# Performance work log

Measured on AMD Instinct MI355X. Metric: run time of the kernel, lower is better.

## Reference

```python
import jax, jax.numpy as jnp
import numpy as np

B, T, INPUT_DIM = 4, 2048, 1024
N_HEADS, HEAD_DIM, EMB_DIM = 16, 64, 1024


def setup_inputs() -> dict:
    key = jax.random.key(0)
    ks = jax.random.split(key, 7)
    s = 0.02
    return {
        "k": jax.random.normal(ks[0], (B, T, INPUT_DIM), jnp.float32),
        "q": jax.random.normal(ks[1], (B, T, INPUT_DIM), jnp.float32),
        "v": jax.random.normal(ks[2], (B, T, INPUT_DIM), jnp.float32),
        # weights stored [in, out] (torch Linear applies x @ W.T with W [out,in])
        "w_key": jax.random.normal(ks[3], (INPUT_DIM, N_HEADS * HEAD_DIM), jnp.float32) * s,
        "w_query": jax.random.normal(ks[4], (INPUT_DIM, N_HEADS * HEAD_DIM), jnp.float32) * s,
        "w_value": jax.random.normal(ks[5], (INPUT_DIM, N_HEADS * HEAD_DIM), jnp.float32) * s,
        "w_proj": jax.random.normal(ks[6], (N_HEADS * HEAD_DIM, EMB_DIM), jnp.float32) * s,
    }


def reference(k, q, v, w_key, w_query, w_value, w_proj):
    temperature = np.sqrt(HEAD_DIM).astype(np.float32)
    # projections -> [B, T, H, D]
    kh = (k @ w_key).reshape(B, T, N_HEADS, HEAD_DIM)
    qh = (q @ w_query).reshape(B, T, N_HEADS, HEAD_DIM)
    vh = (v @ w_value).reshape(B, T, N_HEADS, HEAD_DIM)
    # scaled dot-product attention: scores [B, H, T, T]
    scores = jnp.einsum("bqhd,bkhd->bhqk", qh, kh) / temperature
    attn = jax.nn.softmax(scores, axis=-1)
    out = jnp.einsum("bhqk,bkhd->bqhd", attn, vh).reshape(B, T, N_HEADS * HEAD_DIM)
    return out @ w_proj
```

## Files before the change

kernel.cpp:

```cpp
#include <hip/hip_runtime.h>

typedef unsigned short bf16_t;
typedef __attribute__((ext_vector_type(8))) short short8;
typedef __attribute__((ext_vector_type(4))) float f32x4;
typedef __attribute__((ext_vector_type(16))) float f32x16;
typedef __attribute__((ext_vector_type(4))) unsigned short usx4;

#define T_SEQ 2048
#define NHEAD 16

__device__ __forceinline__ unsigned short f2bf(float x) {
  union { float f; unsigned u; } v; v.f = x;
  unsigned r = v.u + 0x7fffu + ((v.u >> 16) & 1u);
  return (unsigned short)(r >> 16);
}

__device__ __forceinline__ void gld_lds16(const void* g, void* l) {
  __builtin_amdgcn_global_load_lds((const __attribute__((address_space(1))) void*)g,
                                   (__attribute__((address_space(3))) void*)l, 16, 0, 0);
}

__global__ __launch_bounds__(256) void cvt_bf16(const float* __restrict__ in,
                                                bf16_t* __restrict__ out, int n4) {
  int i = blockIdx.x * 256 + threadIdx.x;
  const int stride = gridDim.x * 256;
  for (; i < n4; i += stride) {
    const float4 v = ((const float4*)in)[i];
    usx4 w = { f2bf(v.x), f2bf(v.y), f2bf(v.z), f2bf(v.w) };
    ((usx4*)out)[i] = w;
  }
}

__global__ __launch_bounds__(256) void wtrans(const float* __restrict__ w0, const float* __restrict__ w1,
                                              const float* __restrict__ w2, const float* __restrict__ w3,
                                              bf16_t* __restrict__ wt) {
  __shared__ float tile[32][33];
  const float* w = (blockIdx.z == 0) ? w0 : (blockIdx.z == 1) ? w1 : (blockIdx.z == 2) ? w2 : w3;
  bf16_t* o = wt + (size_t)blockIdx.z * 1024 * 1024;
  const int c = threadIdx.x & 31;
  const int r = threadIdx.x >> 5;
  const int k0 = blockIdx.y * 32, n0 = blockIdx.x * 32;
#pragma unroll
  for (int rr = 0; rr < 32; rr += 8)
    tile[r + rr][c] = w[(size_t)(k0 + r + rr) * 1024 + n0 + c];
  __syncthreads();
#pragma unroll
  for (int rr = 0; rr < 32; rr += 8)
    o[(size_t)(n0 + r + rr) * 1024 + k0 + c] = f2bf(tile[c][r + rr]);
}

template<int MODE>
__global__ __launch_bounds__(256) void gemm128(const bf16_t* __restrict__ A,
                                               const bf16_t* __restrict__ Bt,
                                               void* __restrict__ Cout, int K) {
  __shared__ bf16_t As[128 * 64];
  __shared__ bf16_t Bs[128 * 64];
  const int tid = threadIdx.x;
  const int lane = tid & 63;
  const int l15 = lane & 15;
  const int g = lane >> 4;
  const int wave = tid >> 6;
  const int wr = wave >> 1, wc = wave & 1;
  const int row0 = blockIdx.y * 128, col0 = blockIdx.x * 128;

  f32x4 acc[4][4];
#pragma unroll
  for (int m = 0; m < 4; ++m)
#pragma unroll
    for (int n = 0; n < 4; ++n) acc[m][n] = (f32x4){0.f, 0.f, 0.f, 0.f};

  const int r_st = tid >> 3;
  const int c_st = tid & 7;

  for (int kt = 0; kt < K; kt += 64) {
#pragma unroll
    for (int i = 0; i < 4; ++i) {
      const int r = r_st + i * 32;
      gld_lds16(A  + (size_t)(row0 + r) * K + kt + c_st * 8, As + (size_t)(tid + i * 256) * 8);
      gld_lds16(Bt + (size_t)(col0 + r) * K + kt + c_st * 8, Bs + (size_t)(tid + i * 256) * 8);
    }
    __syncthreads();
#pragma unroll
    for (int ks = 0; ks < 2; ++ks) {
      short8 a[4], b[4];
#pragma unroll
      for (int m = 0; m < 4; ++m)
        a[m] = *(const short8*)(As + (wr * 64 + m * 16 + l15) * 64 + ks * 32 + g * 8);
#pragma unroll
      for (int n = 0; n < 4; ++n)
        b[n] = *(const short8*)(Bs + (wc * 64 + n * 16 + l15) * 64 + ks * 32 + g * 8);
#pragma unroll
      for (int m = 0; m < 4; ++m)
#pragma unroll
        for (int n = 0; n < 4; ++n)
          acc[m][n] = __builtin_amdgcn_mfma_f32_16x16x32_bf16(a[m], b[n], acc[m][n], 0, 0, 0);
    }
    __syncthreads();
  }

  if constexpr (MODE == 0 || MODE == 1) {
    const float sc = (MODE == 1) ? 0.18033688011112042f : 1.0f;
    bf16_t* C = (bf16_t*)Cout;
#pragma unroll
    for (int m = 0; m < 4; ++m) {
      const int row = row0 + wr * 64 + m * 16 + g * 4;
#pragma unroll
      for (int n = 0; n < 4; ++n) {
        const int col = col0 + wc * 64 + n * 16 + l15;
#pragma unroll
        for (int i = 0; i < 4; ++i)
          C[(size_t)(row + i) * 1024 + col] = f2bf(acc[m][n][i] * sc);
      }
    }
  } else if constexpr (MODE == 2) {
    bf16_t* C = (bf16_t*)Cout;
#pragma unroll
    for (int m = 0; m < 4; ++m) {
      const int row = row0 + wr * 64 + m * 16 + g * 4;
      const int bb = row >> 11;
      const int t = row & 2047;
#pragma unroll
      for (int n = 0; n < 4; ++n) {
        const int col = col0 + wc * 64 + n * 16 + l15;
        const int hh = col >> 6, dd = col & 63;
        usx4 w = { f2bf(acc[m][n][0]), f2bf(acc[m][n][1]), f2bf(acc[m][n][2]), f2bf(acc[m][n][3]) };
        *(usx4*)(C + (((size_t)(bb * 16 + hh) * 64 + dd) * 2048 + t)) = w;
      }
    }
  } else {
    float* C = (float*)Cout;
#pragma unroll
    for (int m = 0; m < 4; ++m) {
      const int row = row0 + wr * 64 + m * 16 + g * 4;
#pragma unroll
      for (int n = 0; n < 4; ++n) {
        const int col = col0 + wc * 64 + n * 16 + l15;
#pragma unroll
        for (int i = 0; i < 4; ++i)
          C[(size_t)(row + i) * 1024 + col] = acc[m][n][i];
      }
    }
  }
}

__global__ __launch_bounds__(256) void attn_fwd(const bf16_t* __restrict__ qh,
                                                const bf16_t* __restrict__ kh,
                                                const bf16_t* __restrict__ vt,
                                                bf16_t* __restrict__ ao) {
  __shared__ bf16_t smem[8192];
  bf16_t* Ks = smem;
  bf16_t* Vs = smem + 4096;
  const int tid = threadIdx.x;
  const int lane = tid & 63;
  const int l31 = lane & 31;
  const int half = lane >> 5;
  const int wave = tid >> 6;
  const int qblk = blockIdx.x;
  const int bh = blockIdx.y;
  const int b = bh >> 4, h = bh & 15;

  const int tq = qblk * 128 + wave * 32 + l31;
  const size_t qoff = (size_t)(b * T_SEQ + tq) * 1024 + h * 64;
  short8 qf[4];
#pragma unroll
  for (int ks = 0; ks < 4; ++ks)
    qf[ks] = *(const short8*)(qh + qoff + ks * 16 + half * 8);

  f32x16 ov0, ov1;
#pragma unroll
  for (int i = 0; i < 16; ++i) { ov0[i] = 0.f; ov1[i] = 0.f; }
  float mrun = -1e30f, lrun = 0.f;

  const size_t kbase = (size_t)b * T_SEQ * 1024 + h * 64;
  const size_t vbase = (size_t)bh * 64 * T_SEQ;
  const int r_st = tid >> 3;
  const int cd = tid & 7;

  for (int kv = 0; kv < T_SEQ / 64; ++kv) {
    const int t0 = kv * 64;
#pragma unroll
    for (int i = 0; i < 2; ++i) {
      const int r = r_st + i * 32;
      const int cs = cd ^ (r & 7);
      gld_lds16(kh + kbase + (size_t)(t0 + r) * 1024 + cs * 8, Ks + (size_t)(tid + i * 256) * 8);
      gld_lds16(vt + vbase + (size_t)r * T_SEQ + t0 + cs * 8,  Vs + (size_t)(tid + i * 256) * 8);
    }
    __syncthreads();

    f32x16 st[2];
    __builtin_amdgcn_s_setprio(1);
#pragma unroll
    for (int t = 0; t < 2; ++t) {
#pragma unroll
      for (int i = 0; i < 16; ++i) st[t][i] = 0.f;
      const int row = t * 32 + l31;
#pragma unroll
      for (int ks = 0; ks < 4; ++ks) {
        const short8 af = *(const short8*)(Ks + row * 64 + (((ks * 2 + half) ^ (l31 & 7)) * 8));
        st[t] = __builtin_amdgcn_mfma_f32_32x32x16_bf16(af, qf[ks], st[t], 0, 0, 0);
      }
    }
    __builtin_amdgcn_s_setprio(0);

    float pm = st[0][0];
#pragma unroll
    for (int i = 1; i < 16; ++i) pm = fmaxf(pm, st[0][i]);
#pragma unroll
    for (int i = 0; i < 16; ++i) pm = fmaxf(pm, st[1][i]);
    pm = fmaxf(pm, __shfl_xor(pm, 32));

    if (__any(pm > mrun + 8.f)) {
      const float newm = fmaxf(mrun, pm);
      const float corr = __builtin_amdgcn_exp2f(mrun - newm);
      mrun = newm;
      lrun *= corr;
#pragma unroll
      for (int i = 0; i < 16; ++i) { ov0[i] *= corr; ov1[i] *= corr; }
    }

    float psum = 0.f;
#pragma unroll
    for (int t = 0; t < 2; ++t)
#pragma unroll
      for (int i = 0; i < 16; ++i) {
        const float p = __builtin_amdgcn_exp2f(st[t][i] - mrun);
        st[t][i] = p;
        psum += p;
      }
    psum += __shfl_xor(psum, 32);
    lrun += psum;

#pragma unroll
    for (int s = 0; s < 4; ++s) {
      const int t = s >> 1, base = (s & 1) * 8;
      unsigned c0, c1, c2, c3;
      asm("v_cvt_pk_bf16_f32 %0, %1, %2" : "=v"(c0) : "v"(st[t][base + 0]), "v"(st[t][base + 1]));
      asm("v_cvt_pk_bf16_f32 %0, %1, %2" : "=v"(c1) : "v"(st[t][base + 2]), "v"(st[t][base + 3]));
      asm("v_cvt_pk_bf16_f32 %0, %1, %2" : "=v"(c2) : "v"(st[t][base + 4]), "v"(st[t][base + 5]));
      asm("v_cvt_pk_bf16_f32 %0, %1, %2" : "=v"(c3) : "v"(st[t][base + 6]), "v"(st[t][base + 7]));
      asm("v_permlane32_swap_b32 %0, %1" : "+v"(c0), "+v"(c2));
      asm("v_permlane32_swap_b32 %0, %1" : "+v"(c1), "+v"(c3));
      union { short8 v; unsigned u[4]; } bu;
      bu.u[0] = c0; bu.u[1] = c1; bu.u[2] = c2; bu.u[3] = c3;
      __builtin_amdgcn_s_setprio(1);
#pragma unroll
      for (int dt = 0; dt < 2; ++dt) {
        const int row = dt * 32 + l31;
        const short8 av = *(const short8*)(Vs + row * 64 + (((s * 2 + half) ^ (l31 & 7)) * 8));
        if (dt == 0) ov0 = __builtin_amdgcn_mfma_f32_32x32x16_bf16(av, bu.v, ov0, 0, 0, 0);
        else         ov1 = __builtin_amdgcn_mfma_f32_32x32x16_bf16(av, bu.v, ov1, 0, 0, 0);
      }
      __builtin_amdgcn_s_setprio(0);
    }
    __syncthreads();
  }

  const float inv = 1.f / lrun;
  bf16_t* obuf = smem + wave * 2048;
#pragma unroll
  for (int k = 0; k < 4; ++k) {
    usx4 w0 = { f2bf(ov0[4 * k + 0] * inv), f2bf(ov0[4 * k + 1] * inv),
                f2bf(ov0[4 * k + 2] * inv), f2bf(ov0[4 * k + 3] * inv) };
    *(usx4*)(obuf + l31 * 64 + ((k ^ (l31 & 7)) * 8) + half * 4) = w0;
    usx4 w1 = { f2bf(ov1[4 * k + 0] * inv), f2bf(ov1[4 * k + 1] * inv),
                f2bf(ov1[4 * k + 2] * inv), f2bf(ov1[4 * k + 3] * inv) };
    *(usx4*)(obuf + l31 * 64 + (((4 + k) ^ (l31 & 7)) * 8) + half * 4) = w1;
  }
  __syncthreads();
  const int r = lane >> 1;
  const int cb = (lane & 1) * 4;
  const size_t orow = (size_t)(b * T_SEQ + qblk * 128 + wave * 32 + r) * 1024 + h * 64;
#pragma unroll
  for (int c = 0; c < 4; ++c) {
    const int ch = cb + c;
    const short8 v = *(const short8*)(obuf + r * 64 + ((ch ^ (r & 7)) * 8));
    *(short8*)(ao + orow + ch * 8) = v;
  }
}

extern "C" void kernel_launch(void* const* d_in, const int* in_sizes, int n_in,
                              void* d_out, int out_size, void* d_ws, size_t ws_size,
                              hipStream_t stream) {
  const float* k_in  = (const float*)d_in[0];
  const float* q_in  = (const float*)d_in[1];
  const float* v_in  = (const float*)d_in[2];
  const float* w_key = (const float*)d_in[3];
  const float* w_qry = (const float*)d_in[4];
  const float* w_val = (const float*)d_in[5];
  const float* w_prj = (const float*)d_in[6];

  char* ws = (char*)d_ws;
  bf16_t* xb = (bf16_t*)(ws);
  bf16_t* wt = (bf16_t*)(ws + (16u << 20));
  bf16_t* qh = (bf16_t*)(ws + (24u << 20));
  bf16_t* kh = (bf16_t*)(ws + (40u << 20));
  bf16_t* vt = (bf16_t*)(ws + (56u << 20));
  bf16_t* ao = (bf16_t*)(ws + (72u << 20));

  wtrans<<<dim3(32, 32, 4), 256, 0, stream>>>(w_key, w_qry, w_val, w_prj, wt);

  const int N4 = (8192 * 1024) / 4;
  cvt_bf16<<<2048, 256, 0, stream>>>(k_in, xb, N4);
  gemm128<0><<<dim3(8, 64), 256, 0, stream>>>(xb, wt + 0 * (1u << 20), kh, 1024);
  cvt_bf16<<<2048, 256, 0, stream>>>(q_in, xb, N4);
  gemm128<1><<<dim3(8, 64), 256, 0, stream>>>(xb, wt + 1 * (1u << 20), qh, 1024);
  cvt_bf16<<<2048, 256, 0, stream>>>(v_in, xb, N4);
  gemm128<2><<<dim3(8, 64), 256, 0, stream>>>(xb, wt + 2 * (1u << 20), vt, 1024);

  attn_fwd<<<dim3(16, 64), 256, 0, stream>>>(qh, kh, vt, ao);

  gemm128<3><<<dim3(8, 64), 256, 0, stream>>>(ao, wt + 3 * (1u << 20), d_out, 1024);
}
```

Baseline: 252.4 us.

## Process two query tiles per wave and double-buffer K/V tiles in attention

Each wave now handles 64 query rows (two 32-row groups) against the same K/V tile loaded into LDS, which halves K/V global traffic and LDS fragment loads per query. The grid shrinks to 8 query blocks per head. K/V staging becomes double-buffered, so the next tile's loads overlap the current tile's compute. The running max is folded into the score accumulator initialisation, so scores come out already shifted and no separate subtraction is needed. The cost is more VGPRs (four output accumulators, two Q fragment sets) and double the LDS, which may lower occupancy, plus fewer blocks to spread across CUs.

```diff
diff --git a/kernel.cpp b/kernel.cpp
--- a/kernel.cpp
+++ b/kernel.cpp
@@ -18,6 +18,12 @@
 __device__ __forceinline__ void gld_lds16(const void* g, void* l) {
   __builtin_amdgcn_global_load_lds((const __attribute__((address_space(1))) void*)g,
                                    (__attribute__((address_space(3))) void*)l, 16, 0, 0);
+}
+
+__device__ __forceinline__ unsigned cvtpk(float lo, float hi) {
+  unsigned r;
+  asm("v_cvt_pk_bf16_f32 %0, %1, %2" : "=v"(r) : "v"(lo), "v"(hi));
+  return r;
 }
 
 __global__ __launch_bounds__(256) void cvt_bf16(const float* __restrict__ in,
@@ -147,9 +153,7 @@
                                                 const bf16_t* __restrict__ kh,
                                                 const bf16_t* __restrict__ vt,
                                                 bf16_t* __restrict__ ao) {
-  __shared__ bf16_t smem[8192];
-  bf16_t* Ks = smem;
-  bf16_t* Vs = smem + 4096;
+  __shared__ bf16_t smem[16384];
   const int tid = threadIdx.x;
   const int lane = tid & 63;
   const int l31 = lane & 31;
@@ -159,25 +163,29 @@
   const int bh = blockIdx.y;
   const int b = bh >> 4, h = bh & 15;
 
-  const int tq = qblk * 128 + wave * 32 + l31;
-  const size_t qoff = (size_t)(b * T_SEQ + tq) * 1024 + h * 64;
-  short8 qf[4];
-#pragma unroll
-  for (int ks = 0; ks < 4; ++ks)
-    qf[ks] = *(const short8*)(qh + qoff + ks * 16 + half * 8);
-
-  f32x16 ov0, ov1;
-#pragma unroll
-  for (int i = 0; i < 16; ++i) { ov0[i] = 0.f; ov1[i] = 0.f; }
-  float mrun = -1e30f, lrun = 0.f;
+  const int tqA = qblk * 256 + wave * 64 + l31;
+  const size_t qoffA = (size_t)(b * T_SEQ + tqA) * 1024 + h * 64;
+  short8 qfA[4], qfB[4];
+#pragma unroll
+  for (int ks = 0; ks < 4; ++ks) {
+    qfA[ks] = *(const short8*)(qh + qoffA + ks * 16 + half * 8);
+    qfB[ks] = *(const short8*)(qh + qoffA + 32 * 1024 + ks * 16 + half * 8);
+  }
+
+  f32x16 ovA0, ovA1, ovB0, ovB1;
+#pragma unroll
+  for (int i = 0; i < 16; ++i) { ovA0[i] = 0.f; ovA1[i] = 0.f; ovB0[i] = 0.f; ovB1[i] = 0.f; }
+  float mA = 0.f, lA = 0.f, mB = 0.f, lB = 0.f;
 
   const size_t kbase = (size_t)b * T_SEQ * 1024 + h * 64;
   const size_t vbase = (size_t)bh * 64 * T_SEQ;
   const int r_st = tid >> 3;
   const int cd = tid & 7;
 
-  for (int kv = 0; kv < T_SEQ / 64; ++kv) {
-    const int t0 = kv * 64;
+  auto stage = [&](int kvt, int bufi) {
+    bf16_t* Ks = smem + bufi * 8192;
+    bf16_t* Vs = Ks + 4096;
+    const int t0 = kvt * 64;
 #pragma unroll
     for (int i = 0; i < 2; ++i) {
       const int r = r_st + i * 32;
@@ -185,96 +193,186 @@
       gld_lds16(kh + kbase + (size_t)(t0 + r) * 1024 + cs * 8, Ks + (size_t)(tid + i * 256) * 8);
       gld_lds16(vt + vbase + (size_t)r * T_SEQ + t0 + cs * 8,  Vs + (size_t)(tid + i * 256) * 8);
     }
-    __syncthreads();
-
-    f32x16 st[2];
+  };
+
+  stage(0, 0);
+  __syncthreads();
+
+  for (int kv = 0; kv < T_SEQ / 64; ++kv) {
+    const int cur = kv & 1;
+    if (kv + 1 < T_SEQ / 64) stage(kv + 1, cur ^ 1);
+    const bf16_t* Ks = smem + cur * 8192;
+    const bf16_t* Vs = Ks + 4096;
+
+    f32x16 sA[2], sB[2];
+    const float negmA = -mA, negmB = -mB;
+#pragma unroll
+    for (int t = 0; t < 2; ++t)
+#pragma unroll
+      for (int i = 0; i < 16; ++i) { sA[t][i] = negmA; sB[t][i] = negmB; }
     __builtin_amdgcn_s_setprio(1);
 #pragma unroll
     for (int t = 0; t < 2; ++t) {
-#pragma unroll
-      for (int i = 0; i < 16; ++i) st[t][i] = 0.f;
       const int row = t * 32 + l31;
 #pragma unroll
       for (int ks = 0; ks < 4; ++ks) {
         const short8 af = *(const short8*)(Ks + row * 64 + (((ks * 2 + half) ^ (l31 & 7)) * 8));
-        st[t] = __builtin_amdgcn_mfma_f32_32x32x16_bf16(af, qf[ks], st[t], 0, 0, 0);
+        sA[t] = __builtin_amdgcn_mfma_f32_32x32x16_bf16(af, qfA[ks], sA[t], 0, 0, 0);
+        sB[t] = __builtin_amdgcn_mfma_f32_32x32x16_bf16(af, qfB[ks], sB[t], 0, 0, 0);
       }
     }
     __builtin_amdgcn_s_setprio(0);
 
-    float pm = st[0][0];
-#pragma unroll
-    for (int i = 1; i < 16; ++i) pm = fmaxf(pm, st[0][i]);
-#pragma unroll
-    for (int i = 0; i < 16; ++i) pm = fmaxf(pm, st[1][i]);
-    pm = fmaxf(pm, __shfl_xor(pm, 32));
-
-    if (__any(pm > mrun + 8.f)) {
-      const float newm = fmaxf(mrun, pm);
-      const float corr = __builtin_amdgcn_exp2f(mrun - newm);
-      mrun = newm;
-      lrun *= corr;
-#pragma unroll
-      for (int i = 0; i < 16; ++i) { ov0[i] *= corr; ov1[i] *= corr; }
-    }
-
-    float psum = 0.f;
-#pragma unroll
-    for (int t = 0; t < 2; ++t)
-#pragma unroll
-      for (int i = 0; i < 16; ++i) {
-        const float p = __builtin_amdgcn_exp2f(st[t][i] - mrun);
-        st[t][i] = p;
-        psum += p;
-      }
-    psum += __shfl_xor(psum, 32);
-    lrun += psum;
+    {
+      float pa = fmaxf(sA[0][0], sA[0][1]);
+      float pb = fmaxf(sA[0][2], sA[0][3]);
+#pragma unroll
+      for (int i = 4; i < 16; i += 4) {
+        pa = fmaxf(fmaxf(pa, sA[0][i]), sA[0][i + 1]);
+        pb = fmaxf(fmaxf(pb, sA[0][i + 2]), sA[0][i + 3]);
+      }
+#pragma unroll
+      for (int i = 0; i < 16; i += 4) {
+        pa = fmaxf(fmaxf(pa, sA[1][i]), sA[1][i + 1]);
+        pb = fmaxf(fmaxf(pb, sA[1][i + 2]), sA[1][i + 3]);
+      }
+      float pm = fmaxf(pa, pb);
+      pm = fmaxf(pm, __shfl_xor(pm, 32));
+      if (__any(pm > 8.f)) {
+        const float delta = fmaxf(pm, 0.f);
+        mA += delta;
+        const float corr = __builtin_amdgcn_exp2f(-delta);
+        lA *= corr;
+#pragma unroll
+        for (int i = 0; i < 16; ++i) { ovA0[i] *= corr; ovA1[i] *= corr; }
+#pragma unroll
+        for (int t = 0; t < 2; ++t)
+#pragma unroll
+          for (int i = 0; i < 16; ++i) sA[t][i] -= delta;
+      }
+      float ps0 = 0.f, ps1 = 0.f;
+#pragma unroll
+      for (int t = 0; t < 2; ++t)
+#pragma unroll
+        for (int i = 0; i < 16; i += 2) {
+          const float p0 = __builtin_amdgcn_exp2f(sA[t][i]);
+          const float p1 = __builtin_amdgcn_exp2f(sA[t][i + 1]);
+          sA[t][i] = p0; sA[t][i + 1] = p1;
+          ps0 += p0; ps1 += p1;
+        }
+      float psum = ps0 + ps1;
+      psum += __shfl_xor(psum, 32);
+      lA += psum;
+    }
+    {
+      float pa = fmaxf(sB[0][0], sB[0][1]);
+      float pb = fmaxf(sB[0][2], sB[0][3]);
+#pragma unroll
+      for (int i = 4; i < 16; i += 4) {
+        pa = fmaxf(fmaxf(pa, sB[0][i]), sB[0][i + 1]);
+        pb = fmaxf(fmaxf(pb, sB[0][i + 2]), sB[0][i + 3]);
+      }
+#pragma unroll
+      for (int i = 0; i < 16; i += 4) {
+        pa = fmaxf(fmaxf(pa, sB[1][i]), sB[1][i + 1]);
+        pb = fmaxf(fmaxf(pb, sB[1][i + 2]), sB[1][i + 3]);
+      }
+      float pm = fmaxf(pa, pb);
+      pm = fmaxf(pm, __shfl_xor(pm, 32));
+      if (__any(pm > 8.f)) {
+        const float delta = fmaxf(pm, 0.f);
+        mB += delta;
+        const float corr = __builtin_amdgcn_exp2f(-delta);
+        lB *= corr;
+#pragma unroll
+        for (int i = 0; i < 16; ++i) { ovB0[i] *= corr; ovB1[i] *= corr; }
+#pragma unroll
+        for (int t = 0; t < 2; ++t)
+#pragma unroll
+          for (int i = 0; i < 16; ++i) sB[t][i] -= delta;
+      }
+      float ps0 = 0.f, ps1 = 0.f;
+#pragma unroll
+      for (int t = 0; t < 2; ++t)
+#pragma unroll
+        for (int i = 0; i < 16; i += 2) {
+          const float p0 = __builtin_amdgcn_exp2f(sB[t][i]);
+          const float p1 = __builtin_amdgcn_exp2f(sB[t][i + 1]);
+          sB[t][i] = p0; sB[t][i + 1] = p1;
+          ps0 += p0; ps1 += p1;
+        }
+      float psum = ps0 + ps1;
+      psum += __shfl_xor(psum, 32);
+      lB += psum;
+    }
 
 #pragma unroll
     for (int s = 0; s < 4; ++s) {
       const int t = s >> 1, base = (s & 1) * 8;
-      unsigned c0, c1, c2, c3;
-      asm("v_cvt_pk_bf16_f32 %0, %1, %2" : "=v"(c0) : "v"(st[t][base + 0]), "v"(st[t][base + 1]));
-      asm("v_cvt_pk_bf16_f32 %0, %1, %2" : "=v"(c1) : "v"(st[t][base + 2]), "v"(st[t][base + 3]));
-      asm("v_cvt_pk_bf16_f32 %0, %1, %2" : "=v"(c2) : "v"(st[t][base + 4]), "v"(st[t][base + 5]));
-      asm("v_cvt_pk_bf16_f32 %0, %1, %2" : "=v"(c3) : "v"(st[t][base + 6]), "v"(st[t][base + 7]));
-      asm("v_permlane32_swap_b32 %0, %1" : "+v"(c0), "+v"(c2));
-      asm("v_permlane32_swap_b32 %0, %1" : "+v"(c1), "+v"(c3));
-      union { short8 v; unsigned u[4]; } bu;
-      bu.u[0] = c0; bu.u[1] = c1; bu.u[2] = c2; bu.u[3] = c3;
+      unsigned a0 = cvtpk(sA[t][base + 0], sA[t][base + 1]);
+      unsigned a1 = cvtpk(sA[t][base + 2], sA[t][base + 3]);
+      unsigned a2 = cvtpk(sA[t][base + 4], sA[t][base + 5]);
+      unsigned a3 = cvtpk(sA[t][base + 6], sA[t][base + 7]);
+      asm("v_permlane32_swap_b32 %0, %1" : "+v"(a0), "+v"(a2));
+      asm("v_permlane32_swap_b32 %0, %1" : "+v"(a1), "+v"(a3));
+      unsigned b0 = cvtpk(sB[t][base + 0], sB[t][base + 1]);
+      unsigned b1 = cvtpk(sB[t][base + 2], sB[t][base + 3]);
+      unsigned b2 = cvtpk(sB[t][base + 4], sB[t][base + 5]);
+      unsigned b3 = cvtpk(sB[t][base + 6], sB[t][base + 7]);
+      asm("v_permlane32_swap_b32 %0, %1" : "+v"(b0), "+v"(b2));
+      asm("v_permlane32_swap_b32 %0, %1" : "+v"(b1), "+v"(b3));
+      union { short8 v; unsigned u[4]; } buA, buB;
+      buA.u[0] = a0; buA.u[1] = a1; buA.u[2] = a2; buA.u[3] = a3;
+      buB.u[0] = b0; buB.u[1] = b1; buB.u[2] = b2; buB.u[3] = b3;
       __builtin_amdgcn_s_setprio(1);
 #pragma unroll
       for (int dt = 0; dt < 2; ++dt) {
         const int row = dt * 32 + l31;
         const short8 av = *(const short8*)(Vs + row * 64 + (((s * 2 + half) ^ (l31 & 7)) * 8));
-        if (dt == 0) ov0 = __builtin_amdgcn_mfma_f32_32x32x16_bf16(av, bu.v, ov0, 0, 0, 0);
-        else         ov1 = __builtin_amdgcn_mfma_f32_32x32x16_bf16(av, bu.v, ov1, 0, 0, 0);
+        if (dt == 0) {
+          ovA0 = __builtin_amdgcn_mfma_f32_32x32x16_bf16(av, buA.v, ovA0, 0, 0, 0);
+          ovB0 = __builtin_amdgcn_mfma_f32_32x32x16_bf16(av, buB.v, ovB0, 0, 0, 0);
+        } else {
+          ovA1 = __builtin_amdgcn_mfma_f32_32x32x16_bf16(av, buA.v, ovA1, 0, 0, 0);
+          ovB1 = __builtin_amdgcn_mfma_f32_32x32x16_bf16(av, buB.v, ovB1, 0, 0, 0);
+        }
       }
       __builtin_amdgcn_s_setprio(0);
     }
     __syncthreads();
   }
 
-  const float inv = 1.f / lrun;
-  bf16_t* obuf = smem + wave * 2048;
+  const float invA = 1.f / lA;
+  const float invB = 1.f / lB;
+  bf16_t* obuf = smem + wave * 4096;
 #pragma unroll
   for (int k = 0; k < 4; ++k) {
-    usx4 w0 = { f2bf(ov0[4 * k + 0] * inv), f2bf(ov0[4 * k + 1] * inv),
-                f2bf(ov0[4 * k + 2] * inv), f2bf(ov0[4 * k + 3] * inv) };
-    *(usx4*)(obuf + l31 * 64 + ((k ^ (l31 & 7)) * 8) + half * 4) = w0;
-    usx4 w1 = { f2bf(ov1[4 * k + 0] * inv), f2bf(ov1[4 * k + 1] * inv),
-                f2bf(ov1[4 * k + 2] * inv), f2bf(ov1[4 * k + 3] * inv) };
-    *(usx4*)(obuf + l31 * 64 + (((4 + k) ^ (l31 & 7)) * 8) + half * 4) = w1;
+    usx4 wa0 = { f2bf(ovA0[4 * k + 0] * invA), f2bf(ovA0[4 * k + 1] * invA),
+                 f2bf(ovA0[4 * k + 2] * invA), f2bf(ovA0[4 * k + 3] * invA) };
+    *(usx4*)(obuf + l31 * 64 + ((k ^ (l31 & 7)) * 8) + half * 4) = wa0;
+    usx4 wa1 = { f2bf(ovA1[4 * k + 0] * invA), f2bf(ovA1[4 * k + 1] * invA),
+                 f2bf(ovA1[4 * k + 2] * invA), f2bf(ovA1[4 * k + 3] * invA) };
+    *(usx4*)(obuf + l31 * 64 + (((4 + k) ^ (l31 & 7)) * 8) + half * 4) = wa1;
+    usx4 wb0 = { f2bf(ovB0[4 * k + 0] * invB), f2bf(ovB0[4 * k + 1] * invB),
+                 f2bf(ovB0[4 * k + 2] * invB), f2bf(ovB0[4 * k + 3] * invB) };
+    *(usx4*)(obuf + (32 + l31) * 64 + ((k ^ (l31 & 7)) * 8) + half * 4) = wb0;
+    usx4 wb1 = { f2bf(ovB1[4 * k + 0] * invB), f2bf(ovB1[4 * k + 1] * invB),
+                 f2bf(ovB1[4 * k + 2] * invB), f2bf(ovB1[4 * k + 3] * invB) };
+    *(usx4*)(obuf + (32 + l31) * 64 + (((4 + k) ^ (l31 & 7)) * 8) + half * 4) = wb1;
   }
   __syncthreads();
   const int r = lane >> 1;
   const int cb = (lane & 1) * 4;
-  const size_t orow = (size_t)(b * T_SEQ + qblk * 128 + wave * 32 + r) * 1024 + h * 64;
-#pragma unroll
-  for (int c = 0; c < 4; ++c) {
-    const int ch = cb + c;
-    const short8 v = *(const short8*)(obuf + r * 64 + ((ch ^ (r & 7)) * 8));
-    *(short8*)(ao + orow + ch * 8) = v;
+#pragma unroll
+  for (int hb = 0; hb < 2; ++hb) {
+    const int rr = r + hb * 32;
+    const size_t orow = (size_t)(b * T_SEQ + qblk * 256 + wave * 64 + rr) * 1024 + h * 64;
+#pragma unroll
+    for (int c = 0; c < 4; ++c) {
+      const int ch = cb + c;
+      const short8 v = *(const short8*)(obuf + rr * 64 + ((ch ^ (rr & 7)) * 8));
+      *(short8*)(ao + orow + ch * 8) = v;
+    }
   }
 }
 
@@ -307,7 +405,7 @@
   cvt_bf16<<<2048, 256, 0, stream>>>(v_in, xb, N4);
   gemm128<2><<<dim3(8, 64), 256, 0, stream>>>(xb, wt + 2 * (1u << 20), vt, 1024);
 
-  attn_fwd<<<dim3(16, 64), 256, 0, stream>>>(qh, kh, vt, ao);
+  attn_fwd<<<dim3(8, 64), 256, 0, stream>>>(qh, kh, vt, ao);
 
   gemm128<3><<<dim3(8, 64), 256, 0, stream>>>(ao, wt + 3 * (1u << 20), d_out, 1024);
 }
```

Result: slower. 279.2 us (+10.6%).
